# Kernel tuning notes

Hardware: AMD Instinct MI355X
Metric: run time of the kernel (lower is better)

## Reference

```python
import jax, jax.numpy as jnp
import numpy as np

H = 16  # num_heads
ROPE_BASE = 10000.0

def _rotate_half(x):
    d = x.shape[-1]
    return jnp.concatenate((-x[..., d // 2:], x[..., :d // 2]), axis=-1)

def setup_inputs() -> dict:
    key = jax.random.key(0)
    ks = jax.random.split(key, 9)
    B, S, E = 4, 2048, 1024
    s = 0.02
    return {
        "x": jax.random.normal(ks[0], (B, S, E), dtype=jnp.float32),
        "wq": jax.random.normal(ks[1], (E, E), dtype=jnp.float32) * s,
        "bq": jax.random.normal(ks[2], (E,), dtype=jnp.float32) * s,
        "wk": jax.random.normal(ks[3], (E, E), dtype=jnp.float32) * s,
        "bk": jax.random.normal(ks[4], (E,), dtype=jnp.float32) * s,
        "wv": jax.random.normal(ks[5], (E, E), dtype=jnp.float32) * s,
        "bv": jax.random.normal(ks[6], (E,), dtype=jnp.float32) * s,
        "wo": jax.random.normal(ks[7], (E, E), dtype=jnp.float32) * s,
        "bo": jax.random.normal(ks[8], (E,), dtype=jnp.float32) * s,
    }

def reference(x, wq, bq, wk, bk, wv, bv, wo, bo):
    B, S, E = x.shape
    D = E // H  # head_dim
    # projections (nn.Linear: x @ W.T + b), then split heads -> (B, H, S, D)
    def proj(w, b):
        return (x @ w.T + b).reshape(B, S, H, D).transpose(0, 2, 1, 3)
    q = proj(wq, bq)
    k = proj(wk, bk)
    v = proj(wv, bv)
    # RoPE: freqs (S, D//2) -> repeat_interleave(2) -> (S, D)
    inv_freq = 1.0 / (ROPE_BASE ** (jnp.arange(0, D, 2, dtype=jnp.float32) / D))
    freqs = jnp.arange(S, dtype=jnp.float32)[:, None] * inv_freq[None, :]
    cos = jnp.repeat(jnp.cos(freqs), 2, axis=-1)[None, None]  # (1,1,S,D)
    sin = jnp.repeat(jnp.sin(freqs), 2, axis=-1)[None, None]
    q = q * cos + _rotate_half(q) * sin
    k = k * cos + _rotate_half(k) * sin
    scale = D ** (-0.5)
    scores = jnp.einsum('bhqd,bhkd->bhqk', q, k) * scale
    attn = jax.nn.softmax(scores, axis=-1)
    out = jnp.einsum('bhqk,bhkd->bhqd', attn, v)  # (B,H,S,D)
    out = out.transpose(0, 2, 1, 3).reshape(B, S, E)
    return out @ wo.T + bo
```

## Files before the change

### kernel.cpp

```cpp
#include <hip/hip_runtime.h>


typedef __attribute__((ext_vector_type(4))) float f32x4;
typedef __attribute__((ext_vector_type(8))) short bfrag;
typedef __attribute__((ext_vector_type(4))) short svec4;
typedef __attribute__((ext_vector_type(2))) unsigned int u32x2;

#define MFMA16(a, b, c) __builtin_amdgcn_mfma_f32_16x16x32_bf16(a, b, c, 0, 0, 0)

__device__ __forceinline__ unsigned short f2bf(float f) {
  unsigned u = __builtin_bit_cast(unsigned, f);
  u += 0x7FFFu + ((u >> 16) & 1u);
  return (unsigned short)(u >> 16);
}

__device__ __forceinline__ void gload16(const void* g, void* l) {
  __builtin_amdgcn_global_load_lds(
      (const __attribute__((address_space(1))) unsigned int*)g,
      (__attribute__((address_space(3))) unsigned int*)l, 16, 0, 0);
}

__global__ __launch_bounds__(256) void prep_kernel(
    const float* __restrict__ x, const float* __restrict__ wq,
    const float* __restrict__ wk, const float* __restrict__ wv,
    const float* __restrict__ wo,
    unsigned short* __restrict__ xb, unsigned short* __restrict__ wqb,
    unsigned short* __restrict__ wkb, unsigned short* __restrict__ wvb,
    unsigned short* __restrict__ wob, float2* __restrict__ rope) {
  const int y = blockIdx.y;
  const int tid = blockIdx.x * blockDim.x + threadIdx.x;
  const int stride = gridDim.x * blockDim.x;
  if (y < 5) {
    const float* src = y == 0 ? x : y == 1 ? wq : y == 2 ? wk : y == 3 ? wv : wo;
    unsigned short* dst = y == 0 ? xb : y == 1 ? wqb : y == 2 ? wkb : y == 3 ? wvb : wob;
    const int n4 = (y == 0 ? (8192 * 1024) : (1024 * 1024)) >> 2;
    for (int i = tid; i < n4; i += stride) {
      float4 v = ((const float4*)src)[i];
      svec4 o;
      o.x = (short)f2bf(v.x); o.y = (short)f2bf(v.y);
      o.z = (short)f2bf(v.z); o.w = (short)f2bf(v.w);
      ((svec4*)dst)[i] = o;
    }
  } else {
    for (int i = tid; i < 2048 * 32; i += stride) {
      int s = i >> 5, f = i & 31;
      float invf = powf(10000.0f, -(float)f * (1.0f / 32.0f));
      float ang = (float)s * invf;
      rope[i] = make_float2(cosf(ang), sinf(ang));
    }
  }
}

__global__ __launch_bounds__(256) void gemm_qkv(
    const unsigned short* __restrict__ Xb,
    const unsigned short* __restrict__ Wq, const unsigned short* __restrict__ Wk,
    const unsigned short* __restrict__ Wv,
    const float* __restrict__ biasq, const float* __restrict__ biask,
    const float* __restrict__ biasv,
    const float2* __restrict__ rope,
    unsigned short* __restrict__ Qo, unsigned short* __restrict__ Ko,
    unsigned short* __restrict__ Vto) {
  const int z = blockIdx.z;
  __shared__ unsigned short As[128 * 64];
  __shared__ unsigned short Bs[128 * 64];
  const int t = threadIdx.x;
  const int lane = t & 63, w = t >> 6;
  const int wr = w >> 1, wc = w & 1;
  const int lc = lane & 15, lr = lane >> 4;

  int m0, n0;
  const unsigned short *Apt, *Bpt;
  if (z == 0)      { m0 = blockIdx.y * 128; n0 = blockIdx.x * 128; Apt = Xb; Bpt = Wq; }
  else if (z == 1) { m0 = blockIdx.y * 128; n0 = blockIdx.x * 128; Apt = Xb; Bpt = Wk; }
  else             { m0 = blockIdx.x * 128; n0 = blockIdx.y * 128; Apt = Wv; Bpt = Xb; }

  const int arow = t >> 3;
  const int acol = ((t & 7) << 3) ^ ((arow & 7) << 3);
  const unsigned short* gA = Apt + (size_t)(m0 + arow) * 1024 + acol;
  const unsigned short* gB = Bpt + (size_t)(n0 + arow) * 1024 + acol;
  unsigned short* lA = As + t * 8;
  unsigned short* lB = Bs + t * 8;

  f32x4 acc[4][4];
#pragma unroll
  for (int m = 0; m < 4; ++m)
#pragma unroll
    for (int n = 0; n < 4; ++n) acc[m][n] = (f32x4){0.f, 0.f, 0.f, 0.f};

  const int rsw = (lc & 7) << 3;

#pragma unroll 1
  for (int kt = 0; kt < 16; ++kt) {
    __syncthreads();
#pragma unroll
    for (int c = 0; c < 4; ++c) {
      gload16(gA + (size_t)c * 32 * 1024, lA + c * 2048);
      gload16(gB + (size_t)c * 32 * 1024, lB + c * 2048);
    }
    gA += 64; gB += 64;
    __syncthreads();
#pragma unroll
    for (int ks = 0; ks < 2; ++ks) {
      bfrag af[4], bfr[4];
#pragma unroll
      for (int i = 0; i < 4; ++i)
        af[i] = *(const bfrag*)(As + (wr * 64 + i * 16 + lc) * 64 + ((ks * 32 + lr * 8) ^ rsw));
#pragma unroll
      for (int i = 0; i < 4; ++i)
        bfr[i] = *(const bfrag*)(Bs + (wc * 64 + i * 16 + lc) * 64 + ((ks * 32 + lr * 8) ^ rsw));
#pragma unroll
      for (int m = 0; m < 4; ++m)
#pragma unroll
        for (int n = 0; n < 4; ++n)
          acc[m][n] = MFMA16(af[m], bfr[n], acc[m][n]);
    }
  }

  if (z < 2) {
    const float* bias = (z == 0) ? biasq : biask;
    unsigned short* dst = (z == 0) ? Qo : Ko;
    const float qs = (z == 0) ? 0.125f * 1.44269504f : 1.0f;
    const int h = (n0 + wc * 64) >> 6;
#pragma unroll
    for (int m = 0; m < 4; ++m) {
#pragma unroll
      for (int r = 0; r < 4; ++r) {
        int row = m0 + wr * 64 + m * 16 + lr * 4 + r;
        int b = row >> 11, s = row & 2047;
        const float2* trow = rope + (s << 5);
        size_t base = ((size_t)((b << 4) + h) * 2048 + s) * 64;
#pragma unroll
        for (int n = 0; n < 2; ++n) {
          int col1 = n0 + wc * 64 + n * 16 + lc;
          int d = n * 16 + lc;
          float a  = acc[m][n][r]     + bias[col1];
          float bb = acc[m][n + 2][r] + bias[col1 + 32];
          float2 t0 = trow[d >> 1];
          float2 t1 = trow[16 + (d >> 1)];
          dst[base + d]      = f2bf((a * t0.x - bb * t0.y) * qs);
          dst[base + d + 32] = f2bf((bb * t1.x + a * t1.y) * qs);
        }
      }
    }
  } else {
#pragma unroll
    for (int m = 0; m < 4; ++m) {
#pragma unroll
      for (int r = 0; r < 4; ++r) {
        int wcol = m0 + wr * 64 + m * 16 + lr * 4 + r;
        float bv = biasv[wcol];
        int h = wcol >> 6, d = wcol & 63;
#pragma unroll
        for (int n = 0; n < 4; ++n) {
          int token = n0 + wc * 64 + n * 16 + lc;
          int b = token >> 11, s = token & 2047;
          Vto[((size_t)((b << 4) + h) * 64 + d) * 2048 + s] = f2bf(acc[m][n][r] + bv);
        }
      }
    }
  }
}

__global__ __launch_bounds__(256) void attn_kernel(
    const unsigned short* __restrict__ Q, const unsigned short* __restrict__ K,
    const unsigned short* __restrict__ Vt, unsigned short* __restrict__ O) {
  __shared__ unsigned short Ks[2][64 * 64];
  __shared__ unsigned short Vs[2][64 * 64];
  __shared__ unsigned short Plds[4][32 * 64];
  const int t = threadIdx.x;
  const int lane = t & 63, w = t >> 6;
  const int lc = lane & 15, lr = lane >> 4;
  const int bid = blockIdx.x;
  const int xcd = bid & 7;
  const int jj = bid >> 3;
  const int bh = xcd * 8 + (jj >> 4);
  const int qb = jj & 15;
  const int q0 = qb * 128 + w * 32;

  const unsigned short* Qp = Q + ((size_t)bh * 2048 + q0 + lc) * 64 + lr * 8;
  bfrag aq00 = *(const bfrag*)Qp;
  bfrag aq01 = *(const bfrag*)(Qp + 32);
  bfrag aq10 = *(const bfrag*)(Qp + 16 * 64);
  bfrag aq11 = *(const bfrag*)(Qp + 16 * 64 + 32);

  f32x4 acc0[4], acc1[4];
#pragma unroll
  for (int n = 0; n < 4; ++n) {
    acc0[n] = (f32x4){0.f, 0.f, 0.f, 0.f};
    acc1[n] = (f32x4){0.f, 0.f, 0.f, 0.f};
  }
  float lsum0 = 0.f, lsum1 = 0.f;

  const unsigned short* Kg = K + (size_t)bh * 2048 * 64;
  const unsigned short* Vg = Vt + (size_t)bh * 64 * 2048;

  unsigned short* Pw = &Plds[w][0];
  const int swz = lc & 7;
  unsigned short* pws0 = Pw + lc * 64 + 4 * (lr & 1);
  unsigned short* pws1 = pws0 + 16 * 64;
  const int rsw = swz << 3;

  const int srow = t >> 3;
  const int scol = ((t & 7) ^ (srow & 7)) << 3;

#define STAGE(bufi, kb_)                                                        \
  {                                                                             \
    gload16(Kg + (size_t)((kb_) + srow) * 64 + scol,        Ks[bufi] + t * 8);  \
    gload16(Kg + (size_t)((kb_) + 32 + srow) * 64 + scol,   Ks[bufi] + 2048 + t * 8); \
    gload16(Vg + (size_t)srow * 2048 + (kb_) + scol,        Vs[bufi] + t * 8);  \
    gload16(Vg + (size_t)(32 + srow) * 2048 + (kb_) + scol, Vs[bufi] + 2048 + t * 8); \
  }

  STAGE(0, 0);
  STAGE(1, 64);
  int cur = 0;

#pragma unroll 1
  for (int kt = 0; kt < 32; ++kt) {
    if (kt < 30) { asm volatile("s_waitcnt vmcnt(4)" ::: "memory"); }
    else         { asm volatile("s_waitcnt vmcnt(0)" ::: "memory"); }
    __builtin_amdgcn_s_barrier();

    const unsigned short* KsC = Ks[cur];
    const unsigned short* VsC = Vs[cur];

    f32x4 sc0[4], sc1[4];
    __builtin_amdgcn_s_setprio(1);
#pragma unroll
    for (int c = 0; c < 4; ++c) {
      const unsigned short* kp = KsC + (c * 16 + lc) * 64;
      bfrag k0 = *(const bfrag*)(kp + ((lr * 8) ^ rsw));
      bfrag k1 = *(const bfrag*)(kp + ((32 + lr * 8) ^ rsw));
      f32x4 z0 = (f32x4){0.f, 0.f, 0.f, 0.f};
      z0 = MFMA16(k0, aq00, z0);
      sc0[c] = MFMA16(k1, aq01, z0);
      f32x4 z1 = (f32x4){0.f, 0.f, 0.f, 0.f};
      z1 = MFMA16(k0, aq10, z1);
      sc1[c] = MFMA16(k1, aq11, z1);
    }
    __builtin_amdgcn_s_setprio(0);

#pragma unroll
    for (int c = 0; c < 4; ++c)
#pragma unroll
      for (int r = 0; r < 4; ++r) {
        sc0[c][r] = __builtin_amdgcn_exp2f(sc0[c][r]);
        sc1[c][r] = __builtin_amdgcn_exp2f(sc1[c][r]);
      }
#pragma unroll
    for (int c = 0; c < 4; ++c) {
      lsum0 += (sc0[c][0] + sc0[c][1]) + (sc0[c][2] + sc0[c][3]);
      lsum1 += (sc1[c][0] + sc1[c][1]) + (sc1[c][2] + sc1[c][3]);
    }

#pragma unroll
    for (int c = 0; c < 4; ++c) {
      int off = ((2 * c + (lr >> 1)) ^ swz) << 3;
      unsigned a0, a1, b0, b1;
      asm("v_cvt_pk_bf16_f32 %0, %1, %2" : "=v"(a0) : "v"(sc0[c][0]), "v"(sc0[c][1]));
      asm("v_cvt_pk_bf16_f32 %0, %1, %2" : "=v"(a1) : "v"(sc0[c][2]), "v"(sc0[c][3]));
      asm("v_cvt_pk_bf16_f32 %0, %1, %2" : "=v"(b0) : "v"(sc1[c][0]), "v"(sc1[c][1]));
      asm("v_cvt_pk_bf16_f32 %0, %1, %2" : "=v"(b1) : "v"(sc1[c][2]), "v"(sc1[c][3]));
      u32x2 p0; p0.x = a0; p0.y = a1;
      u32x2 p1; p1.x = b0; p1.y = b1;
      *(u32x2*)(pws0 + off) = p0;
      *(u32x2*)(pws1 + off) = p1;
    }

    bfrag ap00 = *(const bfrag*)(Pw + lc * 64 + ((lr ^ swz) << 3));
    bfrag ap01 = *(const bfrag*)(Pw + lc * 64 + (((4 + lr) ^ swz) << 3));
    bfrag ap10 = *(const bfrag*)(Pw + (16 + lc) * 64 + ((lr ^ swz) << 3));
    bfrag ap11 = *(const bfrag*)(Pw + (16 + lc) * 64 + (((4 + lr) ^ swz) << 3));

    __builtin_amdgcn_s_setprio(1);
#pragma unroll
    for (int n = 0; n < 4; ++n) {
      const unsigned short* vp = VsC + (n * 16 + lc) * 64;
      bfrag bv0 = *(const bfrag*)(vp + ((lr * 8) ^ rsw));
      bfrag bv1 = *(const bfrag*)(vp + ((32 + lr * 8) ^ rsw));
      acc0[n] = MFMA16(ap00, bv0, acc0[n]);
      acc0[n] = MFMA16(ap01, bv1, acc0[n]);
      acc1[n] = MFMA16(ap10, bv0, acc1[n]);
      acc1[n] = MFMA16(ap11, bv1, acc1[n]);
    }
    __builtin_amdgcn_s_setprio(0);

    __builtin_amdgcn_s_barrier();
    if (kt + 2 < 32) STAGE(cur, (kt + 2) * 64);
    cur ^= 1;
  }
#undef STAGE

  float v0 = lsum0, v1 = lsum1;
  v0 += __shfl_xor(v0, 16); v0 += __shfl_xor(v0, 32);
  v1 += __shfl_xor(v1, 16); v1 += __shfl_xor(v1, 32);
  float inv0[4], inv1[4];
#pragma unroll
  for (int r = 0; r < 4; ++r) {
    inv0[r] = 1.0f / __shfl(v0, lr * 4 + r);
    inv1[r] = 1.0f / __shfl(v1, lr * 4 + r);
  }

  const int b = bh >> 4, h = bh & 15;
#pragma unroll
  for (int r = 0; r < 4; ++r) {
    int s0 = q0 + lr * 4 + r;
    size_t base0 = (((size_t)b * 2048 + s0) * 16 + h) * 64;
    size_t base1 = (((size_t)b * 2048 + s0 + 16) * 16 + h) * 64;
#pragma unroll
    for (int n = 0; n < 4; ++n) {
      O[base0 + n * 16 + lc] = f2bf(acc0[n][r] * inv0[r]);
      O[base1 + n * 16 + lc] = f2bf(acc1[n][r] * inv1[r]);
    }
  }
}

__global__ __launch_bounds__(256) void gemm_out(
    const unsigned short* __restrict__ Ob, const unsigned short* __restrict__ Wo,
    const float* __restrict__ bias, float* __restrict__ out) {
  __shared__ unsigned short As[128 * 64];
  __shared__ unsigned short Bs[128 * 64];
  const int t = threadIdx.x;
  const int lane = t & 63, w = t >> 6;
  const int wr = w >> 1, wc = w & 1;
  const int lc = lane & 15, lr = lane >> 4;
  const int m0 = blockIdx.y * 128, n0 = blockIdx.x * 128;

  const int arow = t >> 3;
  const int acol = ((t & 7) << 3) ^ ((arow & 7) << 3);
  const unsigned short* gA = Ob + (size_t)(m0 + arow) * 1024 + acol;
  const unsigned short* gB = Wo + (size_t)(n0 + arow) * 1024 + acol;
  unsigned short* lA = As + t * 8;
  unsigned short* lB = Bs + t * 8;

  f32x4 acc[4][4];
#pragma unroll
  for (int m = 0; m < 4; ++m)
#pragma unroll
    for (int n = 0; n < 4; ++n) acc[m][n] = (f32x4){0.f, 0.f, 0.f, 0.f};

  const int rsw = (lc & 7) << 3;

#pragma unroll 1
  for (int kt = 0; kt < 16; ++kt) {
    __syncthreads();
#pragma unroll
    for (int c = 0; c < 4; ++c) {
      gload16(gA + (size_t)c * 32 * 1024, lA + c * 2048);
      gload16(gB + (size_t)c * 32 * 1024, lB + c * 2048);
    }
    gA += 64; gB += 64;
    __syncthreads();
#pragma unroll
    for (int ks = 0; ks < 2; ++ks) {
      bfrag af[4], bfr[4];
#pragma unroll
      for (int i = 0; i < 4; ++i)
        af[i] = *(const bfrag*)(As + (wr * 64 + i * 16 + lc) * 64 + ((ks * 32 + lr * 8) ^ rsw));
#pragma unroll
      for (int i = 0; i < 4; ++i)
        bfr[i] = *(const bfrag*)(Bs + (wc * 64 + i * 16 + lc) * 64 + ((ks * 32 + lr * 8) ^ rsw));
#pragma unroll
      for (int m = 0; m < 4; ++m)
#pragma unroll
        for (int n = 0; n < 4; ++n)
          acc[m][n] = MFMA16(af[m], bfr[n], acc[m][n]);
    }
  }
#pragma unroll
  for (int n = 0; n < 4; ++n) {
    int col = n0 + wc * 64 + n * 16 + lc;
    float bv = bias[col];
#pragma unroll
    for (int m = 0; m < 4; ++m) {
#pragma unroll
      for (int r = 0; r < 4; ++r) {
        int row = m0 + wr * 64 + m * 16 + lr * 4 + r;
        out[(size_t)row * 1024 + col] = acc[m][n][r] + bv;
      }
    }
  }
}

extern "C" void kernel_launch(void* const* d_in, const int* in_sizes, int n_in,
                              void* d_out, int out_size, void* d_ws, size_t ws_size,
                              hipStream_t stream) {
  (void)in_sizes; (void)n_in; (void)out_size; (void)ws_size;
  const float* x  = (const float*)d_in[0];
  const float* wq = (const float*)d_in[1];
  const float* bq = (const float*)d_in[2];
  const float* wk = (const float*)d_in[3];
  const float* bk = (const float*)d_in[4];
  const float* wv = (const float*)d_in[5];
  const float* bv = (const float*)d_in[6];
  const float* wo = (const float*)d_in[7];
  const float* bo = (const float*)d_in[8];
  float* out = (float*)d_out;

  char* ws = (char*)d_ws;
  unsigned short* Xb   = (unsigned short*)(ws);
  unsigned short* Wqb  = (unsigned short*)(ws + (16ull << 20));
  unsigned short* Wkb  = (unsigned short*)(ws + (18ull << 20));
  unsigned short* Wvb  = (unsigned short*)(ws + (20ull << 20));
  unsigned short* Wob  = (unsigned short*)(ws + (22ull << 20));
  unsigned short* Qb   = (unsigned short*)(ws + (24ull << 20));
  unsigned short* Kb   = (unsigned short*)(ws + (40ull << 20));
  unsigned short* Vt   = (unsigned short*)(ws + (56ull << 20));
  float2* rope         = (float2*)(ws + (72ull << 20));
  unsigned short* Ob   = Xb;

  prep_kernel<<<dim3(1024, 6), 256, 0, stream>>>(x, wq, wk, wv, wo,
                                                 Xb, Wqb, Wkb, Wvb, Wob, rope);
  gemm_qkv<<<dim3(8, 64, 3), 256, 0, stream>>>(Xb, Wqb, Wkb, Wvb,
                                               bq, bk, bv, rope, Qb, Kb, Vt);
  attn_kernel<<<1024, 256, 0, stream>>>(Qb, Kb, Vt, Ob);
  gemm_out<<<dim3(8, 64), 256, 0, stream>>>(Ob, Wob, bo, out);
}
```

Before: 208.2 us.

## Load K/V fragments directly from global memory in attention, dropping LDS staging

The attention kernel no longer stages K and V tiles into double-buffered shared memory with async global-to-LDS loads and barriers. Each wave now reads its K and V MFMA fragments straight from global memory, relying on the cache for reuse across the four waves. A launch-bounds occupancy hint of 4 blocks per CU is added to exploit the lower LDS footprint. This removes barrier synchronization and LDS traffic but quadruples global/L2 load requests and exposes load latency without explicit prefetch.

```diff
diff --git a/kernel.cpp b/kernel.cpp
--- a/kernel.cpp
+++ b/kernel.cpp
@@ -161,11 +161,9 @@
   }
 }
 
-__global__ __launch_bounds__(256) void attn_kernel(
+__global__ __launch_bounds__(256, 4) void attn_kernel(
     const unsigned short* __restrict__ Q, const unsigned short* __restrict__ K,
     const unsigned short* __restrict__ Vt, unsigned short* __restrict__ O) {
-  __shared__ unsigned short Ks[2][64 * 64];
-  __shared__ unsigned short Vs[2][64 * 64];
   __shared__ unsigned short Plds[4][32 * 64];
   const int t = threadIdx.x;
   const int lane = t & 63, w = t >> 6;
@@ -198,39 +196,18 @@
   const int swz = lc & 7;
   unsigned short* pws0 = Pw + lc * 64 + 4 * (lr & 1);
   unsigned short* pws1 = pws0 + 16 * 64;
-  const int rsw = swz << 3;
-
-  const int srow = t >> 3;
-  const int scol = ((t & 7) ^ (srow & 7)) << 3;
-
-#define STAGE(bufi, kb_)                                                        \
-  {                                                                             \
-    gload16(Kg + (size_t)((kb_) + srow) * 64 + scol,        Ks[bufi] + t * 8);  \
-    gload16(Kg + (size_t)((kb_) + 32 + srow) * 64 + scol,   Ks[bufi] + 2048 + t * 8); \
-    gload16(Vg + (size_t)srow * 2048 + (kb_) + scol,        Vs[bufi] + t * 8);  \
-    gload16(Vg + (size_t)(32 + srow) * 2048 + (kb_) + scol, Vs[bufi] + 2048 + t * 8); \
-  }
-
-  STAGE(0, 0);
-  STAGE(1, 64);
-  int cur = 0;
 
 #pragma unroll 1
   for (int kt = 0; kt < 32; ++kt) {
-    if (kt < 30) { asm volatile("s_waitcnt vmcnt(4)" ::: "memory"); }
-    else         { asm volatile("s_waitcnt vmcnt(0)" ::: "memory"); }
-    __builtin_amdgcn_s_barrier();
-
-    const unsigned short* KsC = Ks[cur];
-    const unsigned short* VsC = Vs[cur];
+    const int kb = kt * 64;
 
     f32x4 sc0[4], sc1[4];
     __builtin_amdgcn_s_setprio(1);
 #pragma unroll
     for (int c = 0; c < 4; ++c) {
-      const unsigned short* kp = KsC + (c * 16 + lc) * 64;
-      bfrag k0 = *(const bfrag*)(kp + ((lr * 8) ^ rsw));
-      bfrag k1 = *(const bfrag*)(kp + ((32 + lr * 8) ^ rsw));
+      const unsigned short* kp = Kg + (size_t)(kb + c * 16 + lc) * 64 + lr * 8;
+      bfrag k0 = *(const bfrag*)kp;
+      bfrag k1 = *(const bfrag*)(kp + 32);
       f32x4 z0 = (f32x4){0.f, 0.f, 0.f, 0.f};
       z0 = MFMA16(k0, aq00, z0);
       sc0[c] = MFMA16(k1, aq01, z0);
@@ -275,21 +252,16 @@
     __builtin_amdgcn_s_setprio(1);
 #pragma unroll
     for (int n = 0; n < 4; ++n) {
-      const unsigned short* vp = VsC + (n * 16 + lc) * 64;
-      bfrag bv0 = *(const bfrag*)(vp + ((lr * 8) ^ rsw));
-      bfrag bv1 = *(const bfrag*)(vp + ((32 + lr * 8) ^ rsw));
+      const unsigned short* vp = Vg + (size_t)(n * 16 + lc) * 2048 + kb + lr * 8;
+      bfrag bv0 = *(const bfrag*)vp;
+      bfrag bv1 = *(const bfrag*)(vp + 32);
       acc0[n] = MFMA16(ap00, bv0, acc0[n]);
       acc0[n] = MFMA16(ap01, bv1, acc0[n]);
       acc1[n] = MFMA16(ap10, bv0, acc1[n]);
       acc1[n] = MFMA16(ap11, bv1, acc1[n]);
     }
     __builtin_amdgcn_s_setprio(0);
-
-    __builtin_amdgcn_s_barrier();
-    if (kt + 2 < 32) STAGE(cur, (kt + 2) * 64);
-    cur ^= 1;
-  }
-#undef STAGE
+  }
 
   float v0 = lsum0, v1 = lsum1;
   v0 += __shfl_xor(v0, 16); v0 += __shfl_xor(v0, 32);
```

Measured after the change: 347.6 us. 1.67x slower.
